# Kernel tuning notes

Measured on AMD Instinct MI355X. Metric: run time of the kernel, lower is better.

## Reference

```python
import jax, jax.numpy as jnp
import numpy as np

FEATURE_DIM = 2048
LABEL_DIM = 80
EMBED_DIM = 512
OUTPUT_DIM = 2048
NUM_EXPERTS = 8
BATCH = 1024
IN_DIM = FEATURE_DIM + EMBED_DIM


def setup_inputs() -> dict:
    key = jax.random.key(0)
    ks = jax.random.split(key, 7)
    features = jax.random.normal(ks[0], (BATCH, FEATURE_DIM), dtype=jnp.float32)
    labels = jax.random.uniform(ks[1], (BATCH, LABEL_DIM), dtype=jnp.float32)
    # learned parameters
    label_embed = jax.random.normal(ks[2], (LABEL_DIM, EMBED_DIM), dtype=jnp.float32)
    gate_w = jax.random.normal(ks[3], (IN_DIM, NUM_EXPERTS), dtype=jnp.float32) * (1.0 / np.sqrt(IN_DIM))
    gate_b = jnp.zeros((NUM_EXPERTS,), dtype=jnp.float32)
    expert_w = jax.random.normal(ks[4], (NUM_EXPERTS, IN_DIM, OUTPUT_DIM), dtype=jnp.float32) * (1.0 / np.sqrt(IN_DIM))
    expert_b = jnp.zeros((NUM_EXPERTS, OUTPUT_DIM), dtype=jnp.float32)
    return {
        "features": features,
        "labels": labels,
        "label_embed": label_embed,
        "gate_w": gate_w,
        "gate_b": gate_b,
        "expert_w": expert_w,
        "expert_b": expert_b,
    }


def reference(features, labels, label_embed, gate_w, gate_b, expert_w, expert_b):
    # labels: [B, L] soft multilabel -> label embedding mix [B, E]
    label_embeds = labels @ label_embed                      # [B, EMBED_DIM]
    combined = jnp.concatenate([features, label_embeds], axis=-1)  # [B, IN_DIM]
    gating = jax.nn.sigmoid(combined @ gate_w + gate_b)      # [B, NUM_EXPERTS]
    # all-experts batched GEMM: [B, IN] x [E, IN, OUT] -> [B, E, OUT]
    expert_out = jnp.einsum('bi,eio->beo', combined, expert_w) + expert_b[None, :, :]
    # gate-weighted reduction over experts
    out = jnp.einsum('be,beo->bo', gating, expert_out)       # [B, OUT]
    return out
```

## Files before the change

### kernel.cpp

```cpp
#include <hip/hip_runtime.h>
#include <hip/hip_bf16.h>

#define BATCH   1024
#define FDIM    2048
#define LDIM    80
#define EDIM    512
#define ODIM    2048
#define NEXP    8
#define INDIM   2560

#define BM      256
#define BN      256
#define BK      64
#define NKT     (INDIM / BK)

typedef __bf16 bf16x8 __attribute__((ext_vector_type(8)));
typedef float  f32x4  __attribute__((ext_vector_type(4)));

__device__ __forceinline__ unsigned int pack2(float lo, float hi) {
    __hip_bfloat162 h = __float22bfloat162_rn(make_float2(lo, hi));
    unsigned int u;
    __builtin_memcpy(&u, &h, 4);
    return u;
}
__device__ __forceinline__ float bf2f(unsigned short h) {
    return __uint_as_float((unsigned int)h << 16);
}
__device__ __forceinline__ void gload_lds16(const void* g, void* l) {
    __builtin_amdgcn_global_load_lds(
        (__attribute__((address_space(1))) void*)g,
        (__attribute__((address_space(3))) void*)l,
        16, 0, 0);
}

#define BAR()       __builtin_amdgcn_s_barrier()
#define SCHED_PIN() __builtin_amdgcn_sched_barrier(0)

#define CW_TK 128
#define CW_TO 64
__global__ __launch_bounds__(256) void convert_w(
    const float* __restrict__ W, unsigned short* __restrict__ Wb)
{
    __shared__ float tile[CW_TK][CW_TO + 4];

    const int t  = threadIdx.x;
    const int o0 = blockIdx.x * CW_TO;
    const int k0 = blockIdx.y * CW_TK;
    const int e  = blockIdx.z;

    const int rl = t & 15;
    const int rr = t >> 4;
    const float* src = W + (size_t)e * ((size_t)INDIM * ODIM)
                         + (size_t)(k0 + rr) * ODIM + o0 + rl * 4;
    #pragma unroll
    for (int p = 0; p < CW_TK / 16; ++p) {
        float4 v = *(const float4*)(src + (size_t)(p * 16) * ODIM);
        *(float4*)&tile[rr + p * 16][rl * 4] = v;
    }
    __syncthreads();

    const int o = t >> 2;
    const int c = t & 3;
    unsigned short* dst = Wb + (size_t)e * ((size_t)ODIM * INDIM)
                             + (size_t)(o0 + o) * INDIM + k0 + c * 32;
    #pragma unroll
    for (int u = 0; u < 4; ++u) {
        const int kb = c * 32 + u * 8;
        unsigned int w0 = pack2(tile[kb + 0][o], tile[kb + 1][o]);
        unsigned int w1 = pack2(tile[kb + 2][o], tile[kb + 3][o]);
        unsigned int w2 = pack2(tile[kb + 4][o], tile[kb + 5][o]);
        unsigned int w3 = pack2(tile[kb + 6][o], tile[kb + 7][o]);
        ((uint4*)dst)[u] = make_uint4(w0, w1, w2, w3);
    }
}

__global__ __launch_bounds__(256) void prep_kernel(
    const float* __restrict__ features, const float* __restrict__ labels,
    const float* __restrict__ label_embed, unsigned short* __restrict__ cb)
{
    const int b0 = blockIdx.x * 4;
    const int t  = threadIdx.x;
    __shared__ float lab[4][LDIM];
    for (int idx = t; idx < 4 * LDIM; idx += 256) {
        lab[idx / LDIM][idx % LDIM] = labels[(size_t)(b0 + idx / LDIM) * LDIM + (idx % LDIM)];
    }
    __syncthreads();

    {
        const int r = t >> 6, c64 = t & 63;
        const float4* F4 = (const float4*)features;
        #pragma unroll
        for (int ch = 0; ch < 8; ++ch) {
            float4 v = F4[(size_t)(b0 + r) * (FDIM / 4) + c64 + 64 * ch];
            uint2 pk;
            pk.x = pack2(v.x, v.y);
            pk.y = pack2(v.z, v.w);
            *(uint2*)(cb + (size_t)(b0 + r) * INDIM + (size_t)(c64 + 64 * ch) * 4) = pk;
        }
    }
    {
        const int j = 2 * t;
        float acc[4][2] = {{0,0},{0,0},{0,0},{0,0}};
        const float2* le2 = (const float2*)label_embed;
        for (int l = 0; l < LDIM; ++l) {
            float2 le = le2[(size_t)l * (EDIM / 2) + t];
            #pragma unroll
            for (int r = 0; r < 4; ++r) {
                float lv = lab[r][l];
                acc[r][0] += lv * le.x;
                acc[r][1] += lv * le.y;
            }
        }
        #pragma unroll
        for (int r = 0; r < 4; ++r) {
            *(unsigned int*)(cb + (size_t)(b0 + r) * INDIM + FDIM + j) = pack2(acc[r][0], acc[r][1]);
        }
    }
}

__global__ __launch_bounds__(256) void gate_kernel(
    const unsigned short* __restrict__ cb, const float* __restrict__ gw,
    const float* __restrict__ gb, float* __restrict__ gating)
{
    const int b = blockIdx.x, t = threadIdx.x;
    float p[NEXP] = {0,0,0,0,0,0,0,0};
    for (int i = t; i < INDIM; i += 256) {
        float c = bf2f(cb[(size_t)b * INDIM + i]);
        const float4* g4 = (const float4*)(gw + (size_t)i * NEXP);
        float4 u = g4[0], v = g4[1];
        p[0] += c * u.x; p[1] += c * u.y; p[2] += c * u.z; p[3] += c * u.w;
        p[4] += c * v.x; p[5] += c * v.y; p[6] += c * v.z; p[7] += c * v.w;
    }
    __shared__ float red[4][NEXP];
    const int lane = t & 63, wave = t >> 6;
    #pragma unroll
    for (int e = 0; e < NEXP; ++e) {
        float v = p[e];
        v += __shfl_down(v, 32); v += __shfl_down(v, 16); v += __shfl_down(v, 8);
        v += __shfl_down(v, 4);  v += __shfl_down(v, 2);  v += __shfl_down(v, 1);
        if (lane == 0) red[wave][e] = v;
    }
    __syncthreads();
    if (t < NEXP) {
        float s = red[0][t] + red[1][t] + red[2][t] + red[3][t] + gb[t];
        gating[(size_t)b * NEXP + t] = 1.0f / (1.0f + __expf(-s));
    }
}

template<bool ATOMIC>
__global__ __launch_bounds__(512, 2) void moe_gemm8(
    const unsigned short* __restrict__ cb, const unsigned short* __restrict__ Wb,
    const float* __restrict__ gating, const float* __restrict__ eb,
    float* __restrict__ dst)
{
    __shared__ unsigned short As0[256 * 64];
    __shared__ unsigned short Bs0[256 * 64];
    __shared__ unsigned short As1[256 * 64];
    __shared__ unsigned short Bs1[256 * 64];

    const int t = threadIdx.x;
    const int lane = t & 63, wave = t >> 6;
    const int n0 = blockIdx.x * BN;
    const int m0 = blockIdx.y * BM;
    const int e  = blockIdx.z;

    const int wmi = wave >> 2;
    const int wni = wave & 3;
    const int wmBase = wmi * 128;
    const int wnBase = wni * 64;
    const int fm = lane & 15, fq = lane >> 4;
    const int fsw = fm & 7;

    const int srow = t >> 3;
    const int scn  = (t & 7) ^ (srow & 7);
    const size_t gOff = (size_t)srow * INDIM + (size_t)scn * 8;
    const unsigned short* aS = cb + (size_t)m0 * INDIM + gOff;
    const unsigned short* bS = Wb + (size_t)e * ((size_t)ODIM * INDIM)
                                  + (size_t)n0 * INDIM + gOff;

    #define STAGE4_A(DST, kt) { _Pragma("unroll") for (int q = 0; q < 4; ++q) \
        gload_lds16(aS + (size_t)q * (64 * INDIM) + (size_t)(kt) * 64, (DST) + q * 4096 + wave * 512); }
    #define STAGE4_B(DST, kt) { _Pragma("unroll") for (int q = 0; q < 4; ++q) \
        gload_lds16(bS + (size_t)q * (64 * INDIM) + (size_t)(kt) * 64, (DST) + q * 4096 + wave * 512); }

    #define PH_READ_A(RA, base) { _Pragma("unroll") for (int mi = 0; mi < 4; ++mi) \
        _Pragma("unroll") for (int ks = 0; ks < 2; ++ks) \
            af[mi][ks] = *(const bf16x8*)((RA) + (wmBase + (base) + mi * 16 + fm) * 64 \
                                               + (((ks * 4 + fq) ^ fsw) * 8)); }
    #define PH_READ_B(BF, RB, base) { _Pragma("unroll") for (int ni = 0; ni < 2; ++ni) \
        _Pragma("unroll") for (int ks = 0; ks < 2; ++ks) \
            BF[ni][ks] = *(const bf16x8*)((RB) + (wnBase + (base) + ni * 16 + fm) * 64 \
                                               + (((ks * 4 + fq) ^ fsw) * 8)); }
    #define MFMA16(AI, AJ, BF) { __builtin_amdgcn_s_setprio(1); \
        _Pragma("unroll") for (int mi = 0; mi < 4; ++mi) \
        _Pragma("unroll") for (int ni = 0; ni < 2; ++ni) \
        _Pragma("unroll") for (int ks = 0; ks < 2; ++ks) \
            acc[(AI) + mi][(AJ) + ni] = __builtin_amdgcn_mfma_f32_16x16x32_bf16( \
                af[mi][ks], BF[ni][ks], acc[(AI) + mi][(AJ) + ni], 0, 0, 0); \
        __builtin_amdgcn_s_setprio(0); }

    f32x4 acc[8][4];
    #pragma unroll
    for (int i = 0; i < 8; ++i)
        #pragma unroll
        for (int j = 0; j < 4; ++j) acc[i][j] = (f32x4){0.f, 0.f, 0.f, 0.f};

    bf16x8 af[4][2], bA[2][2], bB[2][2];

    STAGE4_A(As0, 0); STAGE4_B(Bs0, 0); STAGE4_B(Bs1, 1);
    asm volatile("s_waitcnt vmcnt(4)");
    BAR(); SCHED_PIN();

    #define TILE(kt, RA, RB, OA) { \
         \
        PH_READ_A(RA, 0); \
        PH_READ_B(bA, RB, 0); \
        if ((kt) + 1 < NKT) STAGE4_A(OA, (kt) + 1); \
        BAR(); \
        MFMA16(0, 0, bA); \
        SCHED_PIN(); BAR(); SCHED_PIN(); \
         \
        PH_READ_B(bB, RB, 32); \
        BAR(); \
        MFMA16(0, 2, bB); \
        SCHED_PIN(); BAR(); SCHED_PIN(); \
         \
        PH_READ_A(RA, 64); \
        BAR(); \
        MFMA16(4, 2, bB); \
        SCHED_PIN(); BAR(); SCHED_PIN(); \
         \
        if ((kt) + 2 < NKT) STAGE4_B(RB, (kt) + 2); \
        BAR(); \
        MFMA16(4, 0, bA); \
        SCHED_PIN(); \
        if ((kt) + 2 < NKT) { asm volatile("s_waitcnt vmcnt(4)"); } \
        else                { asm volatile("s_waitcnt vmcnt(0)"); } \
        BAR(); SCHED_PIN(); \
    }

    for (int kt = 0; kt < NKT; kt += 2) {
        TILE(kt,     As0, Bs0, As1);
        TILE(kt + 1, As1, Bs1, As0);
    }
    #undef TILE
    #undef STAGE4_A
    #undef STAGE4_B
    #undef PH_READ_A
    #undef PH_READ_B
    #undef MFMA16

    #pragma unroll
    for (int mi = 0; mi < 8; ++mi) {
        const int grow = m0 + wmBase + mi * 16 + fq * 4;
        const float g0 = gating[(size_t)(grow + 0) * NEXP + e];
        const float g1 = gating[(size_t)(grow + 1) * NEXP + e];
        const float g2 = gating[(size_t)(grow + 2) * NEXP + e];
        const float g3 = gating[(size_t)(grow + 3) * NEXP + e];
        #pragma unroll
        for (int ni = 0; ni < 4; ++ni) {
            const int gcol = n0 + wnBase + ni * 16 + fm;
            const float bias = eb[(size_t)e * ODIM + gcol];
            f32x4 a = acc[mi][ni];
            if (ATOMIC) {
                unsafeAtomicAdd(dst + (size_t)(grow + 0) * ODIM + gcol, g0 * (a.x + bias));
                unsafeAtomicAdd(dst + (size_t)(grow + 1) * ODIM + gcol, g1 * (a.y + bias));
                unsafeAtomicAdd(dst + (size_t)(grow + 2) * ODIM + gcol, g2 * (a.z + bias));
                unsafeAtomicAdd(dst + (size_t)(grow + 3) * ODIM + gcol, g3 * (a.w + bias));
            } else {
                float* pd = dst + ((size_t)e * BATCH + grow) * ODIM + gcol;
                pd[0 * ODIM] = g0 * (a.x + bias);
                pd[1 * ODIM] = g1 * (a.y + bias);
                pd[2 * ODIM] = g2 * (a.z + bias);
                pd[3 * ODIM] = g3 * (a.w + bias);
            }
        }
    }
}

__global__ __launch_bounds__(256) void combine_kernel(
    const float* __restrict__ parts, float* __restrict__ out)
{
    const int idx = blockIdx.x * 256 + threadIdx.x;
    const float4* p = (const float4*)parts;
    float4 s = p[idx];
    #pragma unroll
    for (int e = 1; e < NEXP; ++e) {
        float4 v = p[(size_t)e * (BATCH * ODIM / 4) + idx];
        s.x += v.x; s.y += v.y; s.z += v.z; s.w += v.w;
    }
    ((float4*)out)[idx] = s;
}

__global__ __launch_bounds__(256) void moe_gemm_slow(
    const unsigned short* __restrict__ cb, const float* __restrict__ W,
    const float* __restrict__ gating, const float* __restrict__ eb,
    float* __restrict__ out)
{
    __shared__ unsigned short As[128 * 32];
    __shared__ unsigned short Bs[128 * 32];

    const int t = threadIdx.x;
    const int lane = t & 63, wave = t >> 6;
    const int n0 = blockIdx.x * 128;
    const int m0 = blockIdx.y * 128;
    const int e  = blockIdx.z;

    f32x4 acc[4][4];
    #pragma unroll
    for (int i = 0; i < 4; ++i)
        #pragma unroll
        for (int j = 0; j < 4; ++j) acc[i][j] = (f32x4){0.f, 0.f, 0.f, 0.f};

    const int arow = t >> 2, acg = t & 3;
    const unsigned short* ag0 = cb + (size_t)(m0 + arow) * INDIM + acg * 8;
    unsigned short* al0 = As + wave * 512;
    unsigned short* al1 = As + 2048 + wave * 512;

    const int bg = t & 15;
    const int bu = t >> 4;
    const float* wg = W + (size_t)e * ((size_t)INDIM * ODIM) + (size_t)(2 * bg) * ODIM + n0 + bu * 8;
    unsigned int* bl = (unsigned int*)Bs + bg + bu * 128;

    const int fm = lane & 15, fq = lane >> 4;
    const int wn = (wave & 1) * 64;
    const int wm = (wave >> 1) * 64;

    for (int k0 = 0; k0 < INDIM; k0 += 32) {
        __syncthreads();
        gload_lds16(ag0 + k0, al0);
        gload_lds16(ag0 + (size_t)64 * INDIM + k0, al1);
        const float* wp = wg + (size_t)k0 * ODIM;
        float4 r0a = *(const float4*)(wp);
        float4 r0b = *(const float4*)(wp + 4);
        float4 r1a = *(const float4*)(wp + ODIM);
        float4 r1b = *(const float4*)(wp + ODIM + 4);
        bl[0 * 16] = pack2(r0a.x, r1a.x);
        bl[1 * 16] = pack2(r0a.y, r1a.y);
        bl[2 * 16] = pack2(r0a.z, r1a.z);
        bl[3 * 16] = pack2(r0a.w, r1a.w);
        bl[4 * 16] = pack2(r0b.x, r1b.x);
        bl[5 * 16] = pack2(r0b.y, r1b.y);
        bl[6 * 16] = pack2(r0b.z, r1b.z);
        bl[7 * 16] = pack2(r0b.w, r1b.w);
        __syncthreads();

        bf16x8 af[4], bfr[4];
        #pragma unroll
        for (int mi = 0; mi < 4; ++mi)
            af[mi] = *(const bf16x8*)(As + (wm + mi * 16 + fm) * 32 + fq * 8);
        #pragma unroll
        for (int ni = 0; ni < 4; ++ni)
            bfr[ni] = *(const bf16x8*)(Bs + (wn + ni * 16 + fm) * 32 + fq * 8);
        #pragma unroll
        for (int mi = 0; mi < 4; ++mi)
            #pragma unroll
            for (int ni = 0; ni < 4; ++ni)
                acc[mi][ni] = __builtin_amdgcn_mfma_f32_16x16x32_bf16(af[mi], bfr[ni], acc[mi][ni], 0, 0, 0);
    }

    #pragma unroll
    for (int mi = 0; mi < 4; ++mi) {
        const int grow = m0 + wm + mi * 16 + fq * 4;
        const float g0 = gating[(size_t)(grow + 0) * NEXP + e];
        const float g1 = gating[(size_t)(grow + 1) * NEXP + e];
        const float g2 = gating[(size_t)(grow + 2) * NEXP + e];
        const float g3 = gating[(size_t)(grow + 3) * NEXP + e];
        #pragma unroll
        for (int ni = 0; ni < 4; ++ni) {
            const int gcol = n0 + wn + ni * 16 + fm;
            const float bias = eb[(size_t)e * ODIM + gcol];
            f32x4 a = acc[mi][ni];
            unsafeAtomicAdd(out + (size_t)(grow + 0) * ODIM + gcol, g0 * (a.x + bias));
            unsafeAtomicAdd(out + (size_t)(grow + 1) * ODIM + gcol, g1 * (a.y + bias));
            unsafeAtomicAdd(out + (size_t)(grow + 2) * ODIM + gcol, g2 * (a.z + bias));
            unsafeAtomicAdd(out + (size_t)(grow + 3) * ODIM + gcol, g3 * (a.w + bias));
        }
    }
}

extern "C" void kernel_launch(void* const* d_in, const int* in_sizes, int n_in,
                              void* d_out, int out_size, void* d_ws, size_t ws_size,
                              hipStream_t stream) {
    const float* features    = (const float*)d_in[0];
    const float* labels      = (const float*)d_in[1];
    const float* label_embed = (const float*)d_in[2];
    const float* gate_w      = (const float*)d_in[3];
    const float* gate_b      = (const float*)d_in[4];
    const float* expert_w    = (const float*)d_in[5];
    const float* expert_b    = (const float*)d_in[6];
    float* out = (float*)d_out;

    const size_t wb_bytes = (size_t)NEXP * ODIM * INDIM * 2;
    const size_t cb_bytes = (size_t)BATCH * INDIM * 2;
    const size_t gt_bytes = (size_t)BATCH * NEXP * 4;
    const size_t pt_bytes = (size_t)NEXP * BATCH * ODIM * 4;
    const bool fast  = ws_size >= wb_bytes + cb_bytes + gt_bytes;
    const bool fast2 = ws_size >= wb_bytes + cb_bytes + gt_bytes + pt_bytes;

    if (fast) {
        unsigned short* Wb = (unsigned short*)d_ws;
        unsigned short* cb = (unsigned short*)((char*)d_ws + wb_bytes);
        float* gating = (float*)((char*)d_ws + wb_bytes + cb_bytes);
        float* parts  = (float*)((char*)d_ws + wb_bytes + cb_bytes + gt_bytes);
        convert_w<<<dim3(ODIM / CW_TO, INDIM / CW_TK, NEXP), 256, 0, stream>>>(expert_w, Wb);
        prep_kernel<<<BATCH / 4, 256, 0, stream>>>(features, labels, label_embed, cb);
        gate_kernel<<<BATCH, 256, 0, stream>>>(cb, gate_w, gate_b, gating);
        if (fast2) {
            moe_gemm8<false><<<dim3(ODIM / BN, BATCH / BM, NEXP), 512, 0, stream>>>(cb, Wb, gating, expert_b, parts);
            combine_kernel<<<(BATCH * ODIM / 4) / 256, 256, 0, stream>>>(parts, out);
        } else {
            hipMemsetAsync(d_out, 0, (size_t)BATCH * ODIM * sizeof(float), stream);
            moe_gemm8<true><<<dim3(ODIM / BN, BATCH / BM, NEXP), 512, 0, stream>>>(cb, Wb, gating, expert_b, out);
        }
    } else {
        unsigned short* cb = (unsigned short*)d_ws;
        float* gating = (float*)((char*)d_ws + cb_bytes);
        hipMemsetAsync(d_out, 0, (size_t)BATCH * ODIM * sizeof(float), stream);
        prep_kernel<<<BATCH / 4, 256, 0, stream>>>(features, labels, label_embed, cb);
        gate_kernel<<<BATCH, 256, 0, stream>>>(cb, gate_w, gate_b, gating);
        moe_gemm_slow<<<dim3(ODIM / 128, BATCH / 128, NEXP), 256, 0, stream>>>(cb, expert_w, gating, expert_b, out);
    }
}
```

Measured before the change: 377.3 us.

## Merge weight conversion, prep, and gating into one front kernel

Replaces the three separate launches for expert-weight bf16 conversion, combined-input preparation, and gating with a single kernel whose blocks branch by block index into each role. The gating path now recomputes the label embedding in fp32 from the raw inputs instead of reading the prepared bf16 buffer, which removes its dependency on prep and lets all three stages run concurrently. This cuts launch overhead and the serialization gaps between small kernels, at the cost of some duplicated label-embedding work and gating computed in fp32 rather than from bf16 inputs.

```diff
diff --git a/kernel.cpp b/kernel.cpp
--- a/kernel.cpp
+++ b/kernel.cpp
@@ -38,39 +38,132 @@
 
 #define CW_TK 128
 #define CW_TO 64
-__global__ __launch_bounds__(256) void convert_w(
-    const float* __restrict__ W, unsigned short* __restrict__ Wb)
+#define CW_BLOCKS  ((ODIM / CW_TO) * (INDIM / CW_TK) * NEXP)
+#define PREP_BLOCKS (BATCH / 4)
+#define GATE_BLOCKS (BATCH)
+#define FRONT_BLOCKS (CW_BLOCKS + PREP_BLOCKS + GATE_BLOCKS)
+
+__global__ __launch_bounds__(256) void front_kernel(
+    const float* __restrict__ W, unsigned short* __restrict__ Wb,
+    const float* __restrict__ features, const float* __restrict__ labels,
+    const float* __restrict__ label_embed, unsigned short* __restrict__ cb,
+    const float* __restrict__ gw, const float* __restrict__ gb,
+    float* __restrict__ gating)
 {
-    __shared__ float tile[CW_TK][CW_TO + 4];
-
-    const int t  = threadIdx.x;
-    const int o0 = blockIdx.x * CW_TO;
-    const int k0 = blockIdx.y * CW_TK;
-    const int e  = blockIdx.z;
-
-    const int rl = t & 15;
-    const int rr = t >> 4;
-    const float* src = W + (size_t)e * ((size_t)INDIM * ODIM)
-                         + (size_t)(k0 + rr) * ODIM + o0 + rl * 4;
-    #pragma unroll
-    for (int p = 0; p < CW_TK / 16; ++p) {
-        float4 v = *(const float4*)(src + (size_t)(p * 16) * ODIM);
-        *(float4*)&tile[rr + p * 16][rl * 4] = v;
-    }
-    __syncthreads();
-
-    const int o = t >> 2;
-    const int c = t & 3;
-    unsigned short* dst = Wb + (size_t)e * ((size_t)ODIM * INDIM)
-                             + (size_t)(o0 + o) * INDIM + k0 + c * 32;
-    #pragma unroll
-    for (int u = 0; u < 4; ++u) {
-        const int kb = c * 32 + u * 8;
-        unsigned int w0 = pack2(tile[kb + 0][o], tile[kb + 1][o]);
-        unsigned int w1 = pack2(tile[kb + 2][o], tile[kb + 3][o]);
-        unsigned int w2 = pack2(tile[kb + 4][o], tile[kb + 5][o]);
-        unsigned int w3 = pack2(tile[kb + 6][o], tile[kb + 7][o]);
-        ((uint4*)dst)[u] = make_uint4(w0, w1, w2, w3);
+    __shared__ float smem[CW_TK][CW_TO + 4];
+    const int bid = blockIdx.x;
+    const int t   = threadIdx.x;
+
+    if (bid < CW_BLOCKS) {
+        const int o0 = (bid & 31) * CW_TO;
+        const int k0 = ((bid >> 5) % (INDIM / CW_TK)) * CW_TK;
+        const int e  = bid / ((ODIM / CW_TO) * (INDIM / CW_TK));
+
+        const int rl = t & 15;
+        const int rr = t >> 4;
+        const float* src = W + (size_t)e * ((size_t)INDIM * ODIM)
+                             + (size_t)(k0 + rr) * ODIM + o0 + rl * 4;
+        #pragma unroll
+        for (int p = 0; p < CW_TK / 16; ++p) {
+            float4 v = *(const float4*)(src + (size_t)(p * 16) * ODIM);
+            *(float4*)&smem[rr + p * 16][rl * 4] = v;
+        }
+        __syncthreads();
+
+        const int o = t >> 2;
+        const int c = t & 3;
+        unsigned short* dst = Wb + (size_t)e * ((size_t)ODIM * INDIM)
+                                 + (size_t)(o0 + o) * INDIM + k0 + c * 32;
+        #pragma unroll
+        for (int u = 0; u < 4; ++u) {
+            const int kb = c * 32 + u * 8;
+            unsigned int w0 = pack2(smem[kb + 0][o], smem[kb + 1][o]);
+            unsigned int w1 = pack2(smem[kb + 2][o], smem[kb + 3][o]);
+            unsigned int w2 = pack2(smem[kb + 4][o], smem[kb + 5][o]);
+            unsigned int w3 = pack2(smem[kb + 6][o], smem[kb + 7][o]);
+            ((uint4*)dst)[u] = make_uint4(w0, w1, w2, w3);
+        }
+    } else if (bid < CW_BLOCKS + PREP_BLOCKS) {
+        const int b0 = (bid - CW_BLOCKS) * 4;
+        float (*lab)[LDIM] = (float(*)[LDIM])smem;
+        for (int idx = t; idx < 4 * LDIM; idx += 256) {
+            lab[idx / LDIM][idx % LDIM] = labels[(size_t)(b0 + idx / LDIM) * LDIM + (idx % LDIM)];
+        }
+        __syncthreads();
+        {
+            const int r = t >> 6, c64 = t & 63;
+            const float4* F4 = (const float4*)features;
+            #pragma unroll
+            for (int ch = 0; ch < 8; ++ch) {
+                float4 v = F4[(size_t)(b0 + r) * (FDIM / 4) + c64 + 64 * ch];
+                uint2 pk;
+                pk.x = pack2(v.x, v.y);
+                pk.y = pack2(v.z, v.w);
+                *(uint2*)(cb + (size_t)(b0 + r) * INDIM + (size_t)(c64 + 64 * ch) * 4) = pk;
+            }
+        }
+        {
+            const int j = 2 * t;
+            float acc[4][2] = {{0,0},{0,0},{0,0},{0,0}};
+            const float2* le2 = (const float2*)label_embed;
+            for (int l = 0; l < LDIM; ++l) {
+                float2 le = le2[(size_t)l * (EDIM / 2) + t];
+                #pragma unroll
+                for (int r = 0; r < 4; ++r) {
+                    float lv = lab[r][l];
+                    acc[r][0] += lv * le.x;
+                    acc[r][1] += lv * le.y;
+                }
+            }
+            #pragma unroll
+            for (int r = 0; r < 4; ++r) {
+                *(unsigned int*)(cb + (size_t)(b0 + r) * INDIM + FDIM + j) = pack2(acc[r][0], acc[r][1]);
+            }
+        }
+    } else {
+        const int b = bid - CW_BLOCKS - PREP_BLOCKS;
+        float* labs = (float*)smem;
+        float (*red)[NEXP] = (float(*)[NEXP])((float*)smem + 128);
+        if (t < LDIM) labs[t] = labels[(size_t)b * LDIM + t];
+        __syncthreads();
+
+        float p[NEXP] = {0,0,0,0,0,0,0,0};
+        for (int i = t; i < FDIM; i += 256) {
+            float c = features[(size_t)b * FDIM + i];
+            const float4* g4 = (const float4*)(gw + (size_t)i * NEXP);
+            float4 u = g4[0], v = g4[1];
+            p[0] += c * u.x; p[1] += c * u.y; p[2] += c * u.z; p[3] += c * u.w;
+            p[4] += c * v.x; p[5] += c * v.y; p[6] += c * v.z; p[7] += c * v.w;
+        }
+        float le0 = 0.f, le1 = 0.f;
+        for (int l = 0; l < LDIM; ++l) {
+            float lv = labs[l];
+            le0 += lv * label_embed[(size_t)l * EDIM + t];
+            le1 += lv * label_embed[(size_t)l * EDIM + t + 256];
+        }
+        {
+            const float4* g4 = (const float4*)(gw + (size_t)(FDIM + t) * NEXP);
+            float4 u = g4[0], v = g4[1];
+            p[0] += le0 * u.x; p[1] += le0 * u.y; p[2] += le0 * u.z; p[3] += le0 * u.w;
+            p[4] += le0 * v.x; p[5] += le0 * v.y; p[6] += le0 * v.z; p[7] += le0 * v.w;
+            const float4* g5 = (const float4*)(gw + (size_t)(FDIM + 256 + t) * NEXP);
+            float4 u2 = g5[0], v2 = g5[1];
+            p[0] += le1 * u2.x; p[1] += le1 * u2.y; p[2] += le1 * u2.z; p[3] += le1 * u2.w;
+            p[4] += le1 * v2.x; p[5] += le1 * v2.y; p[6] += le1 * v2.z; p[7] += le1 * v2.w;
+        }
+        const int lane = t & 63, wave = t >> 6;
+        #pragma unroll
+        for (int e = 0; e < NEXP; ++e) {
+            float v = p[e];
+            v += __shfl_down(v, 32); v += __shfl_down(v, 16); v += __shfl_down(v, 8);
+            v += __shfl_down(v, 4);  v += __shfl_down(v, 2);  v += __shfl_down(v, 1);
+            if (lane == 0) red[wave][e] = v;
+        }
+        __syncthreads();
+        if (t < NEXP) {
+            float s = red[0][t] + red[1][t] + red[2][t] + red[3][t] + gb[t];
+            gating[(size_t)b * NEXP + t] = 1.0f / (1.0f + __expf(-s));
+        }
     }
 }
 
@@ -403,9 +496,8 @@
         unsigned short* cb = (unsigned short*)((char*)d_ws + wb_bytes);
         float* gating = (float*)((char*)d_ws + wb_bytes + cb_bytes);
         float* parts  = (float*)((char*)d_ws + wb_bytes + cb_bytes + gt_bytes);
-        convert_w<<<dim3(ODIM / CW_TO, INDIM / CW_TK, NEXP), 256, 0, stream>>>(expert_w, Wb);
-        prep_kernel<<<BATCH / 4, 256, 0, stream>>>(features, labels, label_embed, cb);
-        gate_kernel<<<BATCH, 256, 0, stream>>>(cb, gate_w, gate_b, gating);
+        front_kernel<<<FRONT_BLOCKS, 256, 0, stream>>>(
+            expert_w, Wb, features, labels, label_embed, cb, gate_w, gate_b, gating);
         if (fast2) {
             moe_gemm8<false><<<dim3(ODIM / BN, BATCH / BM, NEXP), 512, 0, stream>>>(cb, Wb, gating, expert_b, parts);
             combine_kernel<<<(BATCH * ODIM / 4) / 256, 256, 0, stream>>>(parts, out);
```

After: 372.1 us. About the same (-1.4%).
